# Kernel tuning notes

Hardware: AMD Instinct MI355X
Metric: run time of the kernel (lower is better)

Reference implementation:

```python
import jax, jax.numpy as jnp
import numpy as np
import math

B, S, D = 8, 2048, 512
H, DH = 8, 64  # heads, head dim

def setup_inputs() -> dict:
    key = jax.random.key(0)
    ks = jax.random.split(key, 13)
    w = 0.02
    return {
        "x_Q": jax.random.normal(ks[0], (B, S, D), jnp.float32),
        "x_K": jax.random.normal(ks[1], (B, S, D), jnp.float32),
        "x_V": jax.random.normal(ks[2], (B, S, D), jnp.float32),
        "Wq": jax.random.normal(ks[3], (H * DH, D), jnp.float32) * w,
        "bq": jnp.zeros((H * DH,), jnp.float32),
        "Wk": jax.random.normal(ks[4], (H * DH, D), jnp.float32) * w,
        "bk": jnp.zeros((H * DH,), jnp.float32),
        "Wv": jax.random.normal(ks[5], (H * DH, D), jnp.float32) * w,
        "bv": jnp.zeros((H * DH,), jnp.float32),
        "Wo": jax.random.normal(ks[6], (D, H * DH), jnp.float32) * w,
        "bo": jnp.zeros((D,), jnp.float32),
        "src_batch_lens": jax.random.randint(ks[7], (B,), 1, S + 1, jnp.int32),
    }

def reference(x_Q, x_K, x_V, Wq, bq, Wk, bk, Wv, bv, Wo, bo, src_batch_lens):
    b, s, _ = x_Q.shape
    # projections (torch Linear: x @ W.T + b), split into heads
    Q = (x_Q @ Wq.T + bq).reshape(b, s, H, DH)
    K = (x_K @ Wk.T + bk).reshape(b, s, H, DH)
    V = (x_V @ Wv.T + bv).reshape(b, s, H, DH)
    scale = 1.0 / math.sqrt(DH)
    # [b, h, q, k] scores
    scores = jnp.einsum('bqhd,bkhd->bhqk', Q * scale, K)
    # padding mask on key positions >= src_batch_lens[i], filled with -1e9
    key_mask = jnp.arange(s)[None, :] >= src_batch_lens[:, None]  # [b, k]
    scores = jnp.where(key_mask[:, None, None, :], -1.0e9, scores)
    attn = jax.nn.softmax(scores, axis=-1)  # dropout p=0.0 -> identity
    ctx = jnp.einsum('bhqk,bkhd->bqhd', attn, V).reshape(b, s, H * DH)
    return ctx @ Wo.T + bo
```

## Files before the change

kernel.cpp:

```cpp
#include <hip/hip_runtime.h>
#include <math.h>

#define NB 8
#define NS 2048
#define ND 512
#define NHH 8
#define NDH 64

typedef __attribute__((ext_vector_type(4))) float f32x4;
typedef __attribute__((ext_vector_type(8))) short bf16x8;
typedef unsigned short ush;

__device__ inline ush f2bf_rne(float f) {
    unsigned u = __float_as_uint(f);
    unsigned r = u + 0x7FFFu + ((u >> 16) & 1u);
    return (ush)(r >> 16);
}
__device__ inline float bf2f(ush h) { return __uint_as_float(((unsigned)h) << 16); }

__device__ inline unsigned cvt_pk_bf16(float lo, float hi) {
    unsigned r;
    asm("v_cvt_pk_bf16_f32 %0, %1, %2" : "=v"(r) : "v"(lo), "v"(hi));
    return r;
}

#if defined(__has_builtin)
#if __has_builtin(__builtin_amdgcn_exp2f)
#define EXP2F(x) __builtin_amdgcn_exp2f(x)
#else
#define EXP2F(x) exp2f(x)
#endif
#else
#define EXP2F(x) exp2f(x)
#endif

#define GLL16(gp, lp) __builtin_amdgcn_global_load_lds( \
    (const __attribute__((address_space(1))) unsigned int*)(gp), \
    (__attribute__((address_space(3))) unsigned int*)(lp), 16, 0, 0)

__global__ __launch_bounds__(256) void conv_w_kernel(
    const float* __restrict__ Wq, const float* __restrict__ Wk,
    const float* __restrict__ Wv, const float* __restrict__ Wo,
    ush* __restrict__ wbf, ush* __restrict__ wo_hi, ush* __restrict__ wo_lo)
{
    const int y = blockIdx.y;
    const int i = (blockIdx.x * 256 + threadIdx.x) * 4;
    if (y < 3) {
        const float* src = (y == 0) ? Wq : (y == 1) ? Wk : Wv;
        const float4 v = *(const float4*)&src[i];
        ushort4 o;
        o.x = f2bf_rne(v.x); o.y = f2bf_rne(v.y);
        o.z = f2bf_rne(v.z); o.w = f2bf_rne(v.w);
        *(ushort4*)&wbf[y * 262144 + i] = o;
    } else {
        const float4 v = *(const float4*)&Wo[i];
        ushort4 hi, lo;
        hi.x = f2bf_rne(v.x); lo.x = f2bf_rne(v.x - bf2f(hi.x));
        hi.y = f2bf_rne(v.y); lo.y = f2bf_rne(v.y - bf2f(hi.y));
        hi.z = f2bf_rne(v.z); lo.z = f2bf_rne(v.z - bf2f(hi.z));
        hi.w = f2bf_rne(v.w); lo.w = f2bf_rne(v.w - bf2f(hi.w));
        *(ushort4*)&wo_hi[i] = hi;
        *(ushort4*)&wo_lo[i] = lo;
    }
}

__global__ __launch_bounds__(256) void conv_x_kernel(
    const float* __restrict__ xq, const float* __restrict__ xk,
    const float* __restrict__ xv,
    ush* __restrict__ xqb, ush* __restrict__ xkb, ush* __restrict__ xvb)
{
    const int y = blockIdx.y;
    const float* src = (y == 0) ? xq : (y == 1) ? xk : xv;
    ush* dst = (y == 0) ? xqb : (y == 1) ? xkb : xvb;
    const size_t i = ((size_t)blockIdx.x * 256 + threadIdx.x) * 4;
    const float4 v = *(const float4*)&src[i];
    uint2 p;
    p.x = cvt_pk_bf16(v.x, v.y);
    p.y = cvt_pk_bf16(v.z, v.w);
    *(uint2*)&dst[i] = p;
}

__global__ __launch_bounds__(256) void qkv_gemm_kernel(
    const ush* __restrict__ xqb, const ush* __restrict__ xkb, const ush* __restrict__ xvb,
    const ush* __restrict__ wbf,
    const float* __restrict__ bq, const float* __restrict__ bk, const float* __restrict__ bv,
    ush* __restrict__ Qb, ush* __restrict__ Kb, ush* __restrict__ VT)
{
    __shared__ ush As[2][4096];
    __shared__ ush Bs[2][4096];

    const int z = blockIdx.z;
    const ush*   XA   = (z == 0) ? xqb : (z == 1) ? xkb : xvb;
    const ush*   W    = wbf + z * 262144;
    const float* bias = (z == 0) ? bq : (z == 1) ? bk : bv;

    const int t = threadIdx.x;
    const int w = t >> 6, l = t & 63;
    const int l15 = l & 15, g = l >> 4;

    const int j = blockIdx.x;
    const int m0 = ((j & 7) + (j >> 5) * 8) * 128;
    const int n0 = ((j >> 3) & 3) * 128;
    const int wm = (w & 1) << 6, wn = (w >> 1) << 6;

    const int srow = l >> 2;
    const int sg   = (l & 3) ^ ((srow + (srow >> 2)) & 3);
    const int fsw  = (g ^ ((l15 + (l15 >> 2)) & 3)) << 3;
    const int c0   = w * 2;

    f32x4 acc[4][4];
    #pragma unroll
    for (int i = 0; i < 4; ++i)
        #pragma unroll
        for (int jj = 0; jj < 4; ++jj) acc[i][jj] = (f32x4)(0.0f);

    auto stage = [&](int bf, int kt) {
        GLL16(&XA[(size_t)(m0 + c0 * 16 + srow) * 512 + kt + sg * 8], &As[bf][c0 * 512 + l * 8]);
        GLL16(&XA[(size_t)(m0 + (c0 + 1) * 16 + srow) * 512 + kt + sg * 8], &As[bf][(c0 + 1) * 512 + l * 8]);
        GLL16(&W[(size_t)(n0 + c0 * 16 + srow) * 512 + kt + sg * 8], &Bs[bf][c0 * 512 + l * 8]);
        GLL16(&W[(size_t)(n0 + (c0 + 1) * 16 + srow) * 512 + kt + sg * 8], &Bs[bf][(c0 + 1) * 512 + l * 8]);
    };

    stage(0, 0);
    __syncthreads();

    for (int ki = 0; ki < 16; ++ki) {
        const int buf = ki & 1;
        if (ki < 15) stage(buf ^ 1, (ki + 1) * 32);

        bf16x8 af[4], bfr[4];
        #pragma unroll
        for (int mi = 0; mi < 4; ++mi)
            af[mi] = *(const bf16x8*)&As[buf][(((w & 1) << 2) + mi) * 512 + l15 * 32 + fsw];
        #pragma unroll
        for (int ni = 0; ni < 4; ++ni)
            bfr[ni] = *(const bf16x8*)&Bs[buf][(((w >> 1) << 2) + ni) * 512 + l15 * 32 + fsw];
        #pragma unroll
        for (int mi = 0; mi < 4; ++mi)
            #pragma unroll
            for (int ni = 0; ni < 4; ++ni)
                acc[mi][ni] = __builtin_amdgcn_mfma_f32_16x16x32_bf16(af[mi], bfr[ni], acc[mi][ni], 0, 0, 0);

        __syncthreads();
    }

    const float qscale = (z == 0) ? 0.18033688011112042f : 1.0f;
    float bnv[4];
    #pragma unroll
    for (int ni = 0; ni < 4; ++ni) bnv[ni] = bias[n0 + wn + ni * 16 + l15];

    if (z < 2) {
        ush* O = (z == 0) ? Qb : Kb;
        #pragma unroll
        for (int mi = 0; mi < 4; ++mi) {
            #pragma unroll
            for (int ni = 0; ni < 4; ++ni) {
                const int n = n0 + wn + ni * 16 + l15;
                const int hh = n >> 6, dh = n & 63;
                const int mb = m0 + wm + mi * 16 + (g << 2);
                const int bi = mb >> 11, s = mb & (NS - 1);
                const size_t base = ((size_t)(bi * 8 + hh) * 2048 + s) * 64 + dh;
                const unsigned u01 = cvt_pk_bf16((acc[mi][ni][0] + bnv[ni]) * qscale,
                                                 (acc[mi][ni][1] + bnv[ni]) * qscale);
                const unsigned u23 = cvt_pk_bf16((acc[mi][ni][2] + bnv[ni]) * qscale,
                                                 (acc[mi][ni][3] + bnv[ni]) * qscale);
                O[base]           = (ush)u01;
                O[base + 64]      = (ush)(u01 >> 16);
                O[base + 128]     = (ush)u23;
                O[base + 192]     = (ush)(u23 >> 16);
            }
        }
    } else {
        #pragma unroll
        for (int mi = 0; mi < 4; ++mi) {
            #pragma unroll
            for (int ni = 0; ni < 4; ++ni) {
                const int n = n0 + wn + ni * 16 + l15;
                const int hh = n >> 6, dh = n & 63;
                const int mb = m0 + wm + mi * 16 + (g << 2);
                const int bi = mb >> 11, s = mb & (NS - 1);
                uint2 pk;
                pk.x = cvt_pk_bf16(acc[mi][ni][0] + bnv[ni], acc[mi][ni][1] + bnv[ni]);
                pk.y = cvt_pk_bf16(acc[mi][ni][2] + bnv[ni], acc[mi][ni][3] + bnv[ni]);
                *(uint2*)&VT[((size_t)(bi * 8 + hh) * 64 + dh) * 2048 + s] = pk;
            }
        }
    }
}

__global__ __launch_bounds__(256) void attn_kernel(
    ush* __restrict__ Qb, const ush* __restrict__ Kb,
    const ush* __restrict__ VT, const int* __restrict__ lens,
    ush* __restrict__ ctx_lo)
{
    __shared__ ush Ps[128 * 72];
    __shared__ ush Vt[2 * 4624];

    const int tid = threadIdx.x;
    const int w = tid >> 6, l = tid & 63;
    const int l15 = l & 15, g = l >> 4;

    const int id = blockIdx.x;

    int Ls[8];
    #pragma unroll
    for (int j = 0; j < 8; ++j) Ls[j] = lens[j];
    const int slot = id >> 7;
    int b = 0;
    #pragma unroll
    for (int bb = 0; bb < 8; ++bb) {
        int r = 0;
        #pragma unroll
        for (int j = 0; j < 8; ++j)
            r += (Ls[j] > Ls[bb]) || (Ls[j] == Ls[bb] && j < bb);
        if (r == slot) b = bb;
    }
    const int h = id & 7, qt = (id >> 3) & 15;
    const int L = Ls[b];
    const int q0 = qt << 7;
    const size_t bh = ((size_t)b * 8 + h) * 2048;

    const ush* qptr = Qb + (bh + q0 + w * 16 + l15) * 64 + g * 8;
    const bf16x8 qfa0 = *(const bf16x8*)(qptr);
    const bf16x8 qfa1 = *(const bf16x8*)(qptr + 32);
    const bf16x8 qfb0 = *(const bf16x8*)(qptr + 64 * 64);
    const bf16x8 qfb1 = *(const bf16x8*)(qptr + 64 * 64 + 32);

    const ush* kbase = Kb + (bh + l15) * 64 + g * 8;

    const int dv = tid >> 2, seg = (tid & 3) << 4;
    const ush* vbase = VT + bh * 64 + (size_t)dv * 2048 + seg;
    const int vt_off = dv * 72 + ((dv >> 4) << 3) + seg;

    ush* psw_a = &Ps[(w * 16 + l15) * 72 + (g << 2)];
    const ush* pp_a = &Ps[(w * 16 + l15) * 72 + g * 8];
    ush* psw_b = psw_a + 64 * 72;
    const ush* pp_b = pp_a + 64 * 72;

    bf16x8 ones;
    #pragma unroll
    for (int j = 0; j < 8; ++j) ones[j] = (short)0x3F80;

    f32x4 oa[4], ob[4];
    f32x4 ola = (f32x4)(0.0f), olb = (f32x4)(0.0f);
    #pragma unroll
    for (int i = 0; i < 4; ++i) { oa[i] = (f32x4)(0.0f); ob[i] = (f32x4)(0.0f); }

    f32x4 spa[4], spb[4];
    const int T = (L + 63) >> 6;

    {
        const uint4 v0 = *(const uint4*)(vbase);
        const uint4 v1 = *(const uint4*)(vbase + 8);
        #pragma unroll
        for (int st = 0; st < 4; ++st) { spa[st] = (f32x4)(0.0f); spb[st] = (f32x4)(0.0f); }
        __builtin_amdgcn_s_setprio(1);
        #pragma unroll
        for (int st = 0; st < 4; ++st) {
            const bf16x8 kf0 = *(const bf16x8*)(kbase + st * 1024);
            const bf16x8 kf1 = *(const bf16x8*)(kbase + st * 1024 + 32);
            spa[st] = __builtin_amdgcn_mfma_f32_16x16x32_bf16(kf0, qfa0, spa[st], 0, 0, 0);
            spa[st] = __builtin_amdgcn_mfma_f32_16x16x32_bf16(kf1, qfa1, spa[st], 0, 0, 0);
            spb[st] = __builtin_amdgcn_mfma_f32_16x16x32_bf16(kf0, qfb0, spb[st], 0, 0, 0);
            spb[st] = __builtin_amdgcn_mfma_f32_16x16x32_bf16(kf1, qfb1, spb[st], 0, 0, 0);
        }
        __builtin_amdgcn_s_setprio(0);
        ush* dst = &Vt[vt_off];
        *(uint4*)dst = v0;
        *(uint4*)(dst + 8) = v1;
        __syncthreads();
    }

    auto finish = [&](const ush* vb, bool masked, int kb0) {
        uint2 pka[4], pkb[4];
        #pragma unroll
        for (int st = 0; st < 4; ++st) {
            float pa[4], pb[4];
            #pragma unroll
            for (int r = 0; r < 4; ++r) {
                float ea = EXP2F(spa[st][r]);
                float eb = EXP2F(spb[st][r]);
                if (masked) {
                    const int key = kb0 + st * 16 + (g << 2) + r;
                    ea = (key < L) ? ea : 0.0f;
                    eb = (key < L) ? eb : 0.0f;
                }
                pa[r] = ea; pb[r] = eb;
            }
            pka[st].x = cvt_pk_bf16(pa[0], pa[1]);
            pka[st].y = cvt_pk_bf16(pa[2], pa[3]);
            pkb[st].x = cvt_pk_bf16(pb[0], pb[1]);
            pkb[st].y = cvt_pk_bf16(pb[2], pb[3]);
        }
        #pragma unroll
        for (int st = 0; st < 4; ++st) {
            *(uint2*)(psw_a + st * 16) = pka[st];
            *(uint2*)(psw_b + st * 16) = pkb[st];
        }
        const bf16x8 pfa0 = *(const bf16x8*)(pp_a);
        const bf16x8 pfa1 = *(const bf16x8*)(pp_a + 32);
        const bf16x8 pfb0 = *(const bf16x8*)(pp_b);
        const bf16x8 pfb1 = *(const bf16x8*)(pp_b + 32);
        __builtin_amdgcn_s_setprio(1);
        ola = __builtin_amdgcn_mfma_f32_16x16x32_bf16(pfa0, ones, ola, 0, 0, 0);
        ola = __builtin_amdgcn_mfma_f32_16x16x32_bf16(pfa1, ones, ola, 0, 0, 0);
        olb = __builtin_amdgcn_mfma_f32_16x16x32_bf16(pfb0, ones, olb, 0, 0, 0);
        olb = __builtin_amdgcn_mfma_f32_16x16x32_bf16(pfb1, ones, olb, 0, 0, 0);
        #pragma unroll
        for (int st2 = 0; st2 < 4; ++st2) {
            const ush* vp = vb + (st2 * 16 + l15) * 72 + (st2 << 3) + g * 8;
            const bf16x8 vf0 = *(const bf16x8*)(vp);
            const bf16x8 vf1 = *(const bf16x8*)(vp + 32);
            oa[st2] = __builtin_amdgcn_mfma_f32_16x16x32_bf16(pfa0, vf0, oa[st2], 0, 0, 0);
            oa[st2] = __builtin_amdgcn_mfma_f32_16x16x32_bf16(pfa1, vf1, oa[st2], 0, 0, 0);
            ob[st2] = __builtin_amdgcn_mfma_f32_16x16x32_bf16(pfb0, vf0, ob[st2], 0, 0, 0);
            ob[st2] = __builtin_amdgcn_mfma_f32_16x16x32_bf16(pfb1, vf1, ob[st2], 0, 0, 0);
        }
        __builtin_amdgcn_s_setprio(0);
    };

    for (int t = 1; t < T; ++t) {
        const int k0 = t << 6;
        bf16x8 kf[8];
        const ush* kp = kbase + (size_t)k0 * 64;
        #pragma unroll
        for (int st = 0; st < 4; ++st) {
            kf[2 * st]     = *(const bf16x8*)(kp + st * 1024);
            kf[2 * st + 1] = *(const bf16x8*)(kp + st * 1024 + 32);
        }
        const uint4 nv0 = *(const uint4*)(vbase + k0);
        const uint4 nv1 = *(const uint4*)(vbase + k0 + 8);

        finish(&Vt[((t & 1) ^ 1) * 4624], false, 0);

        #pragma unroll
        for (int st = 0; st < 4; ++st) { spa[st] = (f32x4)(0.0f); spb[st] = (f32x4)(0.0f); }
        __builtin_amdgcn_s_setprio(1);
        #pragma unroll
        for (int st = 0; st < 4; ++st) {
            spa[st] = __builtin_amdgcn_mfma_f32_16x16x32_bf16(kf[2 * st], qfa0, spa[st], 0, 0, 0);
            spa[st] = __builtin_amdgcn_mfma_f32_16x16x32_bf16(kf[2 * st + 1], qfa1, spa[st], 0, 0, 0);
            spb[st] = __builtin_amdgcn_mfma_f32_16x16x32_bf16(kf[2 * st], qfb0, spb[st], 0, 0, 0);
            spb[st] = __builtin_amdgcn_mfma_f32_16x16x32_bf16(kf[2 * st + 1], qfb1, spb[st], 0, 0, 0);
        }
        __builtin_amdgcn_s_setprio(0);

        ush* dst = &Vt[(t & 1) * 4624 + vt_off];
        *(uint4*)dst = nv0;
        *(uint4*)(dst + 8) = nv1;
        __syncthreads();
    }

    finish(&Vt[((T - 1) & 1) * 4624], true, (T - 1) << 6);

    #pragma unroll
    for (int r = 0; r < 4; ++r) {
        const float inva = 1.0f / ola[r];
        const float invb = 1.0f / olb[r];
        const size_t rowa = bh + q0 + w * 16 + (g << 2) + r;
        const size_t rowb = rowa + 64;
        #pragma unroll
        for (int st2 = 0; st2 < 4; ++st2) {
            const float va = oa[st2][r] * inva;
            const ush ha = f2bf_rne(va);
            Qb[rowa * 64 + st2 * 16 + l15] = ha;
            ctx_lo[rowa * 64 + st2 * 16 + l15] = f2bf_rne(va - bf2f(ha));
            const float vbv = ob[st2][r] * invb;
            const ush hb = f2bf_rne(vbv);
            Qb[rowb * 64 + st2 * 16 + l15] = hb;
            ctx_lo[rowb * 64 + st2 * 16 + l15] = f2bf_rne(vbv - bf2f(hb));
        }
    }
}

__global__ __launch_bounds__(512) void out_gemm_kernel(
    const ush* __restrict__ ctx_hi, const ush* __restrict__ ctx_lo,
    const ush* __restrict__ wo_hi, const ush* __restrict__ wo_lo,
    const float* __restrict__ bo, float* __restrict__ out)
{
    __shared__ ush Ah[2][4096], Al[2][4096], Bh[2][4096], Bl[2][4096];

    const int t = threadIdx.x;
    const int w = t >> 6, l = t & 63;
    const int l15 = l & 15, g = l >> 4;

    const int j = blockIdx.x;
    const int m0 = ((j & 7) + (j >> 5) * 8) * 128;
    const int n0 = ((j >> 3) & 3) * 128;
    const int wm = (w & 1) << 6, wn = (w >> 1) << 5;

    const int srow = l >> 2;
    const int sg   = (l & 3) ^ ((srow + (srow >> 2)) & 3);
    const int fsw  = (g ^ ((l15 + (l15 >> 2)) & 3)) << 3;
    const int c0   = w;

    f32x4 acc[4][2];
    #pragma unroll
    for (int i = 0; i < 4; ++i)
        #pragma unroll
        for (int jj = 0; jj < 2; ++jj) acc[i][jj] = (f32x4)(0.0f);

    auto stage = [&](int bf, int kt) {
        const int c = c0;
        const int m = m0 + c * 16 + srow;
        const int k = kt + sg * 8;
        const size_t ga = ((size_t)((m >> 11) * 8 + (k >> 6)) * 2048 + (m & (NS - 1))) * 64 + (k & 63);
        GLL16(&ctx_hi[ga], &Ah[bf][c * 512 + l * 8]);
        GLL16(&ctx_lo[ga], &Al[bf][c * 512 + l * 8]);
        const size_t gb = (size_t)(n0 + c * 16 + srow) * 512 + kt + sg * 8;
        GLL16(&wo_hi[gb], &Bh[bf][c * 512 + l * 8]);
        GLL16(&wo_lo[gb], &Bl[bf][c * 512 + l * 8]);
    };

    stage(0, 0);
    __syncthreads();

    for (int ki = 0; ki < 16; ++ki) {
        const int buf = ki & 1;
        if (ki < 15) stage(buf ^ 1, (ki + 1) * 32);

        bf16x8 ah[4], al[4], bh4[2], bl4[2];
        #pragma unroll
        for (int mi = 0; mi < 4; ++mi) {
            const int off = (((w & 1) << 2) + mi) * 512 + l15 * 32 + fsw;
            ah[mi] = *(const bf16x8*)&Ah[buf][off];
            al[mi] = *(const bf16x8*)&Al[buf][off];
        }
        #pragma unroll
        for (int ni = 0; ni < 2; ++ni) {
            const int off = (((w >> 1) << 1) + ni) * 512 + l15 * 32 + fsw;
            bh4[ni] = *(const bf16x8*)&Bh[buf][off];
            bl4[ni] = *(const bf16x8*)&Bl[buf][off];
        }
        #pragma unroll
        for (int mi = 0; mi < 4; ++mi)
            #pragma unroll
            for (int ni = 0; ni < 2; ++ni) {
                acc[mi][ni] = __builtin_amdgcn_mfma_f32_16x16x32_bf16(ah[mi], bh4[ni], acc[mi][ni], 0, 0, 0);
                acc[mi][ni] = __builtin_amdgcn_mfma_f32_16x16x32_bf16(al[mi], bh4[ni], acc[mi][ni], 0, 0, 0);
                acc[mi][ni] = __builtin_amdgcn_mfma_f32_16x16x32_bf16(ah[mi], bl4[ni], acc[mi][ni], 0, 0, 0);
            }
        __syncthreads();
    }

    float bov[2];
    #pragma unroll
    for (int ni = 0; ni < 2; ++ni) bov[ni] = bo[n0 + wn + ni * 16 + l15];

    #pragma unroll
    for (int mi = 0; mi < 4; ++mi)
        #pragma unroll
        for (int ni = 0; ni < 2; ++ni) {
            const int n = n0 + wn + ni * 16 + l15;
            #pragma unroll
            for (int r = 0; r < 4; ++r) {
                const int m = m0 + wm + mi * 16 + (g << 2) + r;
                out[(size_t)m * 512 + n] = acc[mi][ni][r] + bov[ni];
            }
        }
}

extern "C" void kernel_launch(void* const* d_in, const int* in_sizes, int n_in,
                              void* d_out, int out_size, void* d_ws, size_t ws_size,
                              hipStream_t stream)
{
    const float* xq   = (const float*)d_in[0];
    const float* xk   = (const float*)d_in[1];
    const float* xv   = (const float*)d_in[2];
    const float* Wq   = (const float*)d_in[3];
    const float* bq   = (const float*)d_in[4];
    const float* Wk   = (const float*)d_in[5];
    const float* bk   = (const float*)d_in[6];
    const float* Wv   = (const float*)d_in[7];
    const float* bv   = (const float*)d_in[8];
    const float* Wo   = (const float*)d_in[9];
    const float* bo   = (const float*)d_in[10];
    const int*   lens = (const int*)d_in[11];
    float* out = (float*)d_out;

    const size_t elems = (size_t)NB * NHH * NS * NDH;
    ush* Qb     = (ush*)d_ws;
    ush* Kb     = Qb + elems;
    ush* VT     = Kb + elems;
    ush* ctx_lo = VT + elems;
    ush* wbf    = ctx_lo + elems;
    ush* wo_hi  = wbf + 3 * 262144;
    ush* wo_lo  = wo_hi + 262144;

    ush* xqb = (ush*)out;
    ush* xkb = xqb + elems;
    ush* xvb = ctx_lo;

    const dim3 blk(256);
    conv_w_kernel<<<dim3(256, 4), blk, 0, stream>>>(Wq, Wk, Wv, Wo, wbf, wo_hi, wo_lo);
    conv_x_kernel<<<dim3(8192, 3), blk, 0, stream>>>(xq, xk, xv, xqb, xkb, xvb);
    qkv_gemm_kernel<<<dim3(512, 1, 3), blk, 0, stream>>>(
        xqb, xkb, xvb, wbf, bq, bk, bv, Qb, Kb, VT);
    attn_kernel<<<dim3(NB * NHH * (NS / 128)), blk, 0, stream>>>(Qb, Kb, VT, lens, ctx_lo);
    out_gemm_kernel<<<dim3(512), dim3(512), 0, stream>>>(Qb, ctx_lo, wo_hi, wo_lo, bo, out);
}
```

Before: 299.5 us.

## Deepen QKV GEMM K-tile, reorder attention block mapping, drop setprio hints

```diff
diff --git a/kernel.cpp b/kernel.cpp
--- a/kernel.cpp
+++ b/kernel.cpp
@@ -86,8 +86,8 @@
     const float* __restrict__ bq, const float* __restrict__ bk, const float* __restrict__ bv,
     ush* __restrict__ Qb, ush* __restrict__ Kb, ush* __restrict__ VT)
 {
-    __shared__ ush As[2][4096];
-    __shared__ ush Bs[2][4096];
+    __shared__ ush As[2][8192];
+    __shared__ ush Bs[2][8192];
 
     const int z = blockIdx.z;
     const ush*   XA   = (z == 0) ? xqb : (z == 1) ? xkb : xvb;
@@ -114,32 +114,41 @@
         #pragma unroll
         for (int jj = 0; jj < 4; ++jj) acc[i][jj] = (f32x4)(0.0f);
 
-    auto stage = [&](int bf, int kt) {
-        GLL16(&XA[(size_t)(m0 + c0 * 16 + srow) * 512 + kt + sg * 8], &As[bf][c0 * 512 + l * 8]);
-        GLL16(&XA[(size_t)(m0 + (c0 + 1) * 16 + srow) * 512 + kt + sg * 8], &As[bf][(c0 + 1) * 512 + l * 8]);
-        GLL16(&W[(size_t)(n0 + c0 * 16 + srow) * 512 + kt + sg * 8], &Bs[bf][c0 * 512 + l * 8]);
-        GLL16(&W[(size_t)(n0 + (c0 + 1) * 16 + srow) * 512 + kt + sg * 8], &Bs[bf][(c0 + 1) * 512 + l * 8]);
+    auto stage32 = [&](int bf, int hh, int kt) {
+        const int lo = hh * 4096;
+        GLL16(&XA[(size_t)(m0 + c0 * 16 + srow) * 512 + kt + sg * 8], &As[bf][lo + c0 * 512 + l * 8]);
+        GLL16(&XA[(size_t)(m0 + (c0 + 1) * 16 + srow) * 512 + kt + sg * 8], &As[bf][lo + (c0 + 1) * 512 + l * 8]);
+        GLL16(&W[(size_t)(n0 + c0 * 16 + srow) * 512 + kt + sg * 8], &Bs[bf][lo + c0 * 512 + l * 8]);
+        GLL16(&W[(size_t)(n0 + (c0 + 1) * 16 + srow) * 512 + kt + sg * 8], &Bs[bf][lo + (c0 + 1) * 512 + l * 8]);
     };
 
-    stage(0, 0);
+    stage32(0, 0, 0);
+    stage32(0, 1, 32);
     __syncthreads();
 
-    for (int ki = 0; ki < 16; ++ki) {
+    for (int ki = 0; ki < 8; ++ki) {
         const int buf = ki & 1;
-        if (ki < 15) stage(buf ^ 1, (ki + 1) * 32);
-
-        bf16x8 af[4], bfr[4];
-        #pragma unroll
-        for (int mi = 0; mi < 4; ++mi)
-            af[mi] = *(const bf16x8*)&As[buf][(((w & 1) << 2) + mi) * 512 + l15 * 32 + fsw];
-        #pragma unroll
-        for (int ni = 0; ni < 4; ++ni)
-            bfr[ni] = *(const bf16x8*)&Bs[buf][(((w >> 1) << 2) + ni) * 512 + l15 * 32 + fsw];
-        #pragma unroll
-        for (int mi = 0; mi < 4; ++mi)
+        if (ki < 7) {
+            stage32(buf ^ 1, 0, (ki + 1) * 64);
+            stage32(buf ^ 1, 1, (ki + 1) * 64 + 32);
+        }
+
+        #pragma unroll
+        for (int hh = 0; hh < 2; ++hh) {
+            const int lo = hh * 4096;
+            bf16x8 af[4], bfr[4];
+            #pragma unroll
+            for (int mi = 0; mi < 4; ++mi)
+                af[mi] = *(const bf16x8*)&As[buf][lo + (((w & 1) << 2) + mi) * 512 + l15 * 32 + fsw];
             #pragma unroll
             for (int ni = 0; ni < 4; ++ni)
-                acc[mi][ni] = __builtin_amdgcn_mfma_f32_16x16x32_bf16(af[mi], bfr[ni], acc[mi][ni], 0, 0, 0);
+                bfr[ni] = *(const bf16x8*)&Bs[buf][lo + (((w >> 1) << 2) + ni) * 512 + l15 * 32 + fsw];
+            #pragma unroll
+            for (int mi = 0; mi < 4; ++mi)
+                #pragma unroll
+                for (int ni = 0; ni < 4; ++ni)
+                    acc[mi][ni] = __builtin_amdgcn_mfma_f32_16x16x32_bf16(af[mi], bfr[ni], acc[mi][ni], 0, 0, 0);
+        }
 
         __syncthreads();
     }
@@ -205,7 +214,7 @@
     int Ls[8];
     #pragma unroll
     for (int j = 0; j < 8; ++j) Ls[j] = lens[j];
-    const int slot = id >> 7;
+    const int slot = id & 7;
     int b = 0;
     #pragma unroll
     for (int bb = 0; bb < 8; ++bb) {
@@ -215,7 +224,7 @@
             r += (Ls[j] > Ls[bb]) || (Ls[j] == Ls[bb] && j < bb);
         if (r == slot) b = bb;
     }
-    const int h = id & 7, qt = (id >> 3) & 15;
+    const int h = (id >> 3) & 7, qt = id >> 6;
     const int L = Ls[b];
     const int q0 = qt << 7;
     const size_t bh = ((size_t)b * 8 + h) * 2048;
@@ -254,7 +263,6 @@
         const uint4 v1 = *(const uint4*)(vbase + 8);
         #pragma unroll
         for (int st = 0; st < 4; ++st) { spa[st] = (f32x4)(0.0f); spb[st] = (f32x4)(0.0f); }
-        __builtin_amdgcn_s_setprio(1);
         #pragma unroll
         for (int st = 0; st < 4; ++st) {
             const bf16x8 kf0 = *(const bf16x8*)(kbase + st * 1024);
@@ -264,7 +272,6 @@
             spb[st] = __builtin_amdgcn_mfma_f32_16x16x32_bf16(kf0, qfb0, spb[st], 0, 0, 0);
             spb[st] = __builtin_amdgcn_mfma_f32_16x16x32_bf16(kf1, qfb1, spb[st], 0, 0, 0);
         }
-        __builtin_amdgcn_s_setprio(0);
         ush* dst = &Vt[vt_off];
         *(uint4*)dst = v0;
         *(uint4*)(dst + 8) = v1;
@@ -301,7 +308,6 @@
         const bf16x8 pfa1 = *(const bf16x8*)(pp_a + 32);
         const bf16x8 pfb0 = *(const bf16x8*)(pp_b);
         const bf16x8 pfb1 = *(const bf16x8*)(pp_b + 32);
-        __builtin_amdgcn_s_setprio(1);
         ola = __builtin_amdgcn_mfma_f32_16x16x32_bf16(pfa0, ones, ola, 0, 0, 0);
         ola = __builtin_amdgcn_mfma_f32_16x16x32_bf16(pfa1, ones, ola, 0, 0, 0);
         olb = __builtin_amdgcn_mfma_f32_16x16x32_bf16(pfb0, ones, olb, 0, 0, 0);
@@ -316,7 +322,6 @@
             ob[st2] = __builtin_amdgcn_mfma_f32_16x16x32_bf16(pfb0, vf0, ob[st2], 0, 0, 0);
             ob[st2] = __builtin_amdgcn_mfma_f32_16x16x32_bf16(pfb1, vf1, ob[st2], 0, 0, 0);
         }
-        __builtin_amdgcn_s_setprio(0);
     };
 
     for (int t = 1; t < T; ++t) {
@@ -335,7 +340,6 @@
 
         #pragma unroll
         for (int st = 0; st < 4; ++st) { spa[st] = (f32x4)(0.0f); spb[st] = (f32x4)(0.0f); }
-        __builtin_amdgcn_s_setprio(1);
         #pragma unroll
         for (int st = 0; st < 4; ++st) {
             spa[st] = __builtin_amdgcn_mfma_f32_16x16x32_bf16(kf[2 * st], qfa0, spa[st], 0, 0, 0);
@@ -343,7 +347,6 @@
             spb[st] = __builtin_amdgcn_mfma_f32_16x16x32_bf16(kf[2 * st], qfb0, spb[st], 0, 0, 0);
             spb[st] = __builtin_amdgcn_mfma_f32_16x16x32_bf16(kf[2 * st + 1], qfb1, spb[st], 0, 0, 0);
         }
-        __builtin_amdgcn_s_setprio(0);
 
         ush* dst = &Vt[(t & 1) * 4624 + vt_off];
         *(uint4*)dst = nv0;
```

After: 379.8 us. 26.8% more time.
